# Kernel tuning notes

Measured on AMD Instinct MI355X. Metric: run time of the kernel, lower is better.

## Reference

```python
import jax, jax.numpy as jnp
import numpy as np
import math

MUL = 32          # multiplicity of 0e and 1o node irreps
NATTR = 4         # node attribute scalars (species one-hot)
NBASIS = 10       # radial basis size
HID = 64          # radial MLP hidden width
RMAX = 4.0
NUM_NEIGHBORS = 32.0
NLAYERS = 2
OUT_DIM = 16
NGRAPH = 8
SQRT3 = math.sqrt(3.0)


def smooth_cutoff(xr):
    u = 2.0 * (xr - 1.0)
    y = (1.0 - jnp.cos(math.pi * u)) * 0.5
    return jnp.where(u > 0.0, 0.0, jnp.where(u < -1.0, 1.0, y))


def fctp(s, v, attr, W0, W1, fan_in):
    # FullyConnectedTensorProduct with scalar attrs: mixes channels u x a -> w.
    norm = 1.0 / math.sqrt(fan_in)
    so = jnp.einsum('nu,na,uaw->nw', s, attr, W0) * norm
    vo = jnp.einsum('nui,na,uaw->nwi', v, attr, W1) * norm
    return so, vo


def setup_inputs() -> dict:
    key = jax.random.key(0)
    ks = jax.random.split(key, 16)
    N, E = 10000, 320000
    x = jax.random.normal(ks[0], (N, MUL * 4), dtype=jnp.float32)  # 32x0e + 32x1o
    node_attr = jax.random.uniform(ks[1], (N, NATTR), dtype=jnp.float32)
    edge_vec = jax.random.normal(ks[2], (E, 3), dtype=jnp.float32)
    edge_src = jax.random.randint(ks[3], (E,), 0, N, dtype=jnp.int32)
    edge_dst = jax.random.randint(ks[4], (E,), 0, N, dtype=jnp.int32)
    batch = jnp.sort(jax.random.randint(ks[5], (N,), 0, NGRAPH, dtype=jnp.int32))
    g = lambda k, shp: jax.random.normal(k, shp, dtype=jnp.float32)
    L = NLAYERS
    return {
        'x': x, 'node_attr': node_attr, 'edge_vec': edge_vec, 'batch': batch,
        'edge_src': edge_src, 'edge_dst': edge_dst,
        'Wsc0': g(ks[6], (L, MUL, NATTR, MUL)),
        'Wsc1': g(ks[7], (L, MUL, NATTR, MUL)),
        'Wl10': g(ks[8], (L, MUL, NATTR, MUL)),
        'Wl11': g(ks[9], (L, MUL, NATTR, MUL)),
        'Wfc1': g(ks[10], (L, NBASIS, HID)),
        'Wfc2': g(ks[11], (L, HID, 4 * MUL)),
        'Wl20': g(ks[12], (L, 2 * MUL, NATTR, MUL)),
        'Wl21': g(ks[13], (L, 2 * MUL, NATTR, MUL)),
        'Wread': g(ks[14], (MUL, NATTR, OUT_DIM)),
    }


def reference(x, node_attr, edge_vec, batch, edge_src, edge_dst,
              Wsc0, Wsc1, Wl10, Wl11, Wfc1, Wfc2, Wl20, Wl21, Wread):
    N = x.shape[0]
    s = x[:, :MUL]                                # [N, 32]  scalars (0e)
    v = x[:, MUL:].reshape(N, MUL, 3)             # [N, 32, 3] vectors (1o)

    # edge geometry -> spherical harmonics (component norm) + radial embedding
    length = jnp.linalg.norm(edge_vec, axis=-1)               # [E]
    unit = edge_vec / (length + 1e-9)[:, None]
    Y1 = SQRT3 * unit                                         # l=1 SH, Y0 == 1
    centers = jnp.linspace(0.0, RMAX, NBASIS)
    emb = jnp.exp(-(((length[:, None] - centers) / (RMAX / NBASIS)) ** 2))
    emb = emb * smooth_cutoff(length / RMAX)[:, None]         # [E, 10]

    c_s, c_x = math.sin(math.pi / 8), math.cos(math.pi / 8)

    for l in range(NLAYERS):
        # self connection and first linear (FCTP with node attrs)
        sc_s, sc_v = fctp(s, v, node_attr, Wsc0[l], Wsc1[l], MUL * NATTR)
        xs, xv = fctp(s, v, node_attr, Wl10[l], Wl11[l], MUL * NATTR)

        # radial MLP -> per-edge 'uvu' tensor-product weights (4 paths x MUL)
        h = jax.nn.silu(emb @ Wfc1[l] / math.sqrt(NBASIS))
        w = (h @ Wfc2[l]) / math.sqrt(HID)
        w = w.reshape(-1, 4, MUL)                             # [E, 4, 32]

        sE = xs[edge_src]                                     # [E, 32]
        vE = xv[edge_src]                                     # [E, 32, 3]
        # CG paths kept by Convolution (out in irreps_out or 0e):
        mid0a = w[:, 0] * sE                                   # 0e x 0e -> 0e
        mid0b = w[:, 1] * jnp.einsum('ei,eui->eu', Y1, vE) / SQRT3  # 1o x 1o -> 0e
        mid1a = w[:, 2][:, :, None] * sE[:, :, None] * Y1[:, None, :]  # 0e x 1o -> 1o
        mid1b = w[:, 3][:, :, None] * vE                       # 1o x 0e -> 1o
        mid_s = jnp.concatenate([mid0a, mid0b], axis=1)        # [E, 64]
        mid_v = jnp.concatenate([mid1a, mid1b], axis=1)        # [E, 64, 3]

        inv = 1.0 / math.sqrt(NUM_NEIGHBORS)
        agg_s = jax.ops.segment_sum(mid_s, edge_dst, num_segments=N) * inv
        agg_v = jax.ops.segment_sum(mid_v, edge_dst, num_segments=N) * inv

        os_, ov = fctp(agg_s, agg_v, node_attr, Wl20[l], Wl21[l], 2 * MUL * NATTR)
        s_new = c_s * sc_s + c_x * os_
        v_new = c_s * sc_v + c_x * ov

        # gate nonlinearity (equivariant) + residual (CustomCompose)
        s = s + jax.nn.silu(s_new)
        v = v + v_new * jax.nn.sigmoid(s_new)[:, :, None]

    # scalar readout + per-graph pooling
    out_node = jnp.einsum('nu,na,uaw->nw', s, node_attr, Wread) / math.sqrt(MUL * NATTR)
    pooled = jax.ops.segment_sum(out_node, batch, num_segments=NGRAPH)
    pooled = pooled / math.sqrt(N / NGRAPH)
    return pooled
```

## Files before the change

kernel.cpp:

```cpp
#include <hip/hip_runtime.h>
#include <math.h>

#define MUL 32
#define NATTR 4
#define NBASIS 10
#define HID 64
#define OUT_DIM 16
#define NGRAPH 8
#define NT 513

#define PI_F 3.14159265358979323846f
#define SQRT3_F 1.7320508075688772f
#define INV_SQRT3_F 0.5773502691896258f
#define INV_SQRT10_F 0.31622776601683794f
#define INV_SQRTNN_F 0.17677669529663687f
#define NORM128_F 0.08838834764831845f
#define NORM256_F 0.0625f
#define C_S_F 0.3826834323650898f
#define C_X_F 0.9238795325112867f
#define CSTEP_F (4.0f/9.0f)

__device__ inline unsigned short f2bf(float x) {
    unsigned u = __float_as_uint(x);
    u += 0x7FFF + ((u >> 16) & 1);
    return (unsigned short)(u >> 16);
}
__device__ inline float bf2f(unsigned short h) {
    return __uint_as_float(((unsigned)h) << 16);
}

__device__ __forceinline__ void init_sv_body(
    int blk, const float* __restrict__ x,
    float* __restrict__ s, float* __restrict__ v, int N) {
    int i = blk * 256 + threadIdx.x;
    if (i >= N * 128) return;
    int n = i >> 7, c = i & 127;
    float val = x[i];
    if (c < 32) s[n * 32 + c] = val;
    else        v[n * 96 + (c - 32)] = val;
}

__device__ __forceinline__ void setup_weights_body(
    int blk,
    const float* __restrict__ Wsc0, const float* __restrict__ Wl10,
    const float* __restrict__ Wsc1, const float* __restrict__ Wl11,
    const float* __restrict__ Wl20, const float* __restrict__ Wl21,
    float* __restrict__ Wfp, unsigned* __restrict__ Wupk) {
    int i = blk * 256 + threadIdx.x;
    if (i < 32768) {
        int idx = i >> 12;
        int r = i & 4095;
        int l = idx >> 2, m = idx & 3;
        const float* base = (m == 0 ? Wsc0 : m == 1 ? Wl10 : m == 2 ? Wsc1 : Wl11)
                            + l * 4096;
        int u = r >> 7, rr = r & 127, a = rr >> 5, ww = rr & 31;
        Wfp[idx * 4096 + u * 128 + ww * 4 + a] = base[r];
    } else if (i < 49152) {
        int j = i - 32768;
        int l = j >> 13;
        int r = j & 8191;
        int u = r >> 7, rr = r & 127, a = rr >> 5, ww = rr & 31;
        unsigned lo = f2bf(Wl20[l * 8192 + r]);
        unsigned hi = f2bf(Wl21[l * 8192 + r]);
        Wupk[l * 8192 + u * 128 + ww * 4 + a] = lo | (hi << 16);
    }
}

__device__ __forceinline__ void tab_gen_body(
    int blk, const float* __restrict__ Wfc1, const float* __restrict__ Wfc2,
    unsigned* __restrict__ tab, float (*sh_h)[64]) {
    int g = threadIdx.x >> 6;
    int n = threadIdx.x & 63;
    int row = blk * 4 + g;
    bool valid = row < 2 * NT;
    int l = valid ? row / NT : 0;
    int i = valid ? row % NT : 0;
    float len = (float)i * (1.0f / 128.0f);
    float uu = len * 0.5f - 2.0f;
    float cut = (uu > 0.0f) ? 0.0f
              : ((uu < -1.0f) ? 1.0f : 0.5f * (1.0f - __cosf(PI_F * uu)));
    const float* W1 = Wfc1 + l * 640;
    float a = 0.f;
#pragma unroll
    for (int k = 0; k < 10; k++) {
        float d = (len - k * CSTEP_F) * 2.5f;
        float e = __expf(-d * d) * cut;
        a += e * W1[k * 64 + n];
    }
    a *= INV_SQRT10_F;
    sh_h[g][n] = a / (1.0f + __expf(-a));
    __syncthreads();
    if (!valid) return;
    const float* W2 = Wfc2 + l * 8192;
    float w0 = 0.f, w1 = 0.f;
#pragma unroll 8
    for (int nn = 0; nn < 64; nn++) {
        float hn = sh_h[g][nn];
        w0 += hn * W2[nn * 128 + n];
        w1 += hn * W2[nn * 128 + 64 + n];
    }
    w0 *= 0.125f; w1 *= 0.125f;
    tab[(size_t)l * NT * 64 + i * 64 + n] =
        (unsigned)f2bf(w0) | ((unsigned)f2bf(w1) << 16);
}

__device__ __forceinline__ void csr_count_body(
    int blk, const int* __restrict__ edst, int* __restrict__ cnt, int E) {
    int e = blk * 256 + threadIdx.x;
    if (e < E) atomicAdd(&cnt[edst[e]], 1);
}

__device__ __forceinline__ void csr_fill_body(
    int blk, const int* __restrict__ edst, const int* __restrict__ esrc,
    const float* __restrict__ edge_vec, int* __restrict__ cursor,
    float* __restrict__ vec_csr, int E) {
    int e = blk * 256 + threadIdx.x;
    if (e < E) {
        int d = edst[e];
        int p = atomicAdd(&cursor[d], 1);
        float4 vv = {edge_vec[e * 3 + 0], edge_vec[e * 3 + 1], edge_vec[e * 3 + 2],
                     __int_as_float(esrc[e])};
        *(float4*)(vec_csr + (size_t)p * 4) = vv;
    }
}

__device__ __forceinline__ void node_fctp_body(
    int blk, int path,
    const float* __restrict__ s, const float* __restrict__ v,
    const float* __restrict__ attr, const float* __restrict__ Wfp,
    float* __restrict__ sc_s, float* __restrict__ sc_v,
    float* __restrict__ xsv, int N, char* smem) {
    float* w0 = (float*)smem;
    float* w1 = (float*)(smem + 16384);
    float (*sh)[96] = (float(*)[96])(smem + 32768);
    int ln = threadIdx.x >> 5, w = threadIdx.x & 31;
    const float4* W0p = (const float4*)(Wfp + path * 8192);
    const float4* W1p = (const float4*)(Wfp + path * 8192 + 4096);
    for (int i = threadIdx.x; i < 1024; i += 256) {
        ((float4*)w0)[i] = W0p[i];
        ((float4*)w1)[i] = W1p[i];
    }
    for (int g = 0; g < 2; g++) {
        int n = blk * 16 + g * 8 + ln;
        bool valid = n < N;
        __syncthreads();
        if (valid) {
            if (path == 0) {
                sh[ln][w] = s[n * 32 + w];
            } else {
                sh[ln][w * 3 + 0] = v[n * 96 + w * 3 + 0];
                sh[ln][w * 3 + 1] = v[n * 96 + w * 3 + 1];
                sh[ln][w * 3 + 2] = v[n * 96 + w * 3 + 2];
            }
        }
        __syncthreads();
        if (!valid) continue;
        float4 at = *(const float4*)(attr + n * 4);
        if (path == 0) {
            float acc0 = 0.f, acc1 = 0.f;
            for (int u = 0; u < 32; u++) {
                float su = sh[ln][u];
                float4 W0v = *(const float4*)(w0 + u * 128 + w * 4);
                float4 W1v = *(const float4*)(w1 + u * 128 + w * 4);
                float d0 = at.x * W0v.x + at.y * W0v.y + at.z * W0v.z + at.w * W0v.w;
                float d1 = at.x * W1v.x + at.y * W1v.y + at.z * W1v.z + at.w * W1v.w;
                acc0 += su * d0;
                acc1 += su * d1;
            }
            sc_s[n * 32 + w] = acc0 * NORM128_F;
            xsv[(size_t)n * 128 + w * 4 + 3] = acc1 * NORM128_F;
        } else {
            float a00 = 0, a01 = 0, a02 = 0, a10 = 0, a11 = 0, a12 = 0;
            for (int u = 0; u < 32; u++) {
                float vu0 = sh[ln][u * 3 + 0];
                float vu1 = sh[ln][u * 3 + 1];
                float vu2 = sh[ln][u * 3 + 2];
                float4 W0v = *(const float4*)(w0 + u * 128 + w * 4);
                float4 W1v = *(const float4*)(w1 + u * 128 + w * 4);
                float d0 = at.x * W0v.x + at.y * W0v.y + at.z * W0v.z + at.w * W0v.w;
                float d1 = at.x * W1v.x + at.y * W1v.y + at.z * W1v.z + at.w * W1v.w;
                a00 += vu0 * d0; a01 += vu1 * d0; a02 += vu2 * d0;
                a10 += vu0 * d1; a11 += vu1 * d1; a12 += vu2 * d1;
            }
            sc_v[n * 96 + w * 3 + 0] = a00 * NORM128_F;
            sc_v[n * 96 + w * 3 + 1] = a01 * NORM128_F;
            sc_v[n * 96 + w * 3 + 2] = a02 * NORM128_F;
            float* xp = xsv + (size_t)n * 128 + w * 4;
            xp[0] = a10 * NORM128_F;
            xp[1] = a11 * NORM128_F;
            xp[2] = a12 * NORM128_F;
        }
    }
}

__device__ __forceinline__ void node_update_body(
    int blk, const float* __restrict__ agg_s, const float* __restrict__ agg_v,
    const float* __restrict__ attr, const unsigned* __restrict__ Wupk,
    const float* __restrict__ sc_s, const float* __restrict__ sc_v,
    float* __restrict__ s, float* __restrict__ v, int N, char* smem) {
    unsigned* pk = (unsigned*)smem;
    float (*sh_as)[64]  = (float(*)[64])(smem + 32768);
    float (*sh_av)[192] = (float(*)[192])(smem + 32768 + 2048);
    int ln = threadIdx.x >> 5, w = threadIdx.x & 31;
    for (int i = threadIdx.x; i < 2048; i += 256)
        ((uint4*)pk)[i] = ((const uint4*)Wupk)[i];
    for (int g = 0; g < 2; g++) {
        int n = blk * 16 + g * 8 + ln;
        bool valid = n < N;
        __syncthreads();
        if (valid) {
            sh_as[ln][w] = agg_s[n * 64 + w];
            sh_as[ln][32 + w] = agg_s[n * 64 + 32 + w];
#pragma unroll
            for (int i = 0; i < 6; i++)
                sh_av[ln][w * 6 + i] = agg_v[(size_t)n * 192 + w * 6 + i];
        }
        __syncthreads();
        if (!valid) continue;
        float4 at = *(const float4*)(attr + n * 4);
        float acc_s = 0.f, a0 = 0.f, a1 = 0.f, a2 = 0.f;
        for (int u = 0; u < 64; u++) {
            float gs = sh_as[ln][u];
            float g0 = sh_av[ln][u * 3 + 0];
            float g1 = sh_av[ln][u * 3 + 1];
            float g2 = sh_av[ln][u * 3 + 2];
            uint4 pv = *(const uint4*)(pk + u * 128 + w * 4);
            float w20x = bf2f((unsigned short)pv.x), w21x = bf2f((unsigned short)(pv.x >> 16));
            float w20y = bf2f((unsigned short)pv.y), w21y = bf2f((unsigned short)(pv.y >> 16));
            float w20z = bf2f((unsigned short)pv.z), w21z = bf2f((unsigned short)(pv.z >> 16));
            float w20w = bf2f((unsigned short)pv.w), w21w = bf2f((unsigned short)(pv.w >> 16));
            float d0 = at.x * w20x + at.y * w20y + at.z * w20z + at.w * w20w;
            float d1 = at.x * w21x + at.y * w21y + at.z * w21z + at.w * w21w;
            acc_s += gs * d0;
            a0 += g0 * d1; a1 += g1 * d1; a2 += g2 * d1;
        }
        float os = acc_s * NORM256_F;
        float sn = C_S_F * sc_s[n * 32 + w] + C_X_F * os;
        float sig = 1.0f / (1.0f + __expf(-sn));
        s[n * 32 + w] += sn * sig;
        float ov0 = a0 * NORM256_F, ov1 = a1 * NORM256_F, ov2 = a2 * NORM256_F;
        v[n * 96 + w * 3 + 0] += (C_S_F * sc_v[n * 96 + w * 3 + 0] + C_X_F * ov0) * sig;
        v[n * 96 + w * 3 + 1] += (C_S_F * sc_v[n * 96 + w * 3 + 1] + C_X_F * ov1) * sig;
        v[n * 96 + w * 3 + 2] += (C_S_F * sc_v[n * 96 + w * 3 + 2] + C_X_F * ov2) * sig;
    }
}

__global__ __launch_bounds__(256) void mega1(
    int nTab, int nInit, int nSetup,
    const float* __restrict__ x, float* __restrict__ s, float* __restrict__ v,
    const float* __restrict__ Wfc1, const float* __restrict__ Wfc2,
    const float* __restrict__ Wsc0, const float* __restrict__ Wl10,
    const float* __restrict__ Wsc1, const float* __restrict__ Wl11,
    const float* __restrict__ Wl20, const float* __restrict__ Wl21,
    float* __restrict__ Wfp, unsigned* __restrict__ Wupk,
    unsigned* __restrict__ tab,
    const int* __restrict__ edst, int* __restrict__ cnt, int N, int E) {
    __shared__ float sh_h[4][64];
    int b = blockIdx.x;
    if (b < nTab) { tab_gen_body(b, Wfc1, Wfc2, tab, sh_h); return; }
    b -= nTab;
    if (b < nInit) { init_sv_body(b, x, s, v, N); return; }
    b -= nInit;
    if (b < nSetup) {
        setup_weights_body(b, Wsc0, Wl10, Wsc1, Wl11, Wl20, Wl21, Wfp, Wupk);
        return;
    }
    b -= nSetup;
    csr_count_body(b, edst, cnt, E);
}

__global__ void csr_scan(const int* __restrict__ cnt, int* __restrict__ off,
                         int* __restrict__ cursor, int N) {
    __shared__ int sums[256];
    int t = threadIdx.x;
    int chunk = (N + 255) / 256;
    int lo = t * chunk, hi = lo + chunk; if (hi > N) hi = N;
    int s = 0;
    for (int i = lo; i < hi; i++) s += cnt[i];
    sums[t] = s;
    __syncthreads();
    for (int d = 1; d < 256; d <<= 1) {
        int v = (t >= d) ? sums[t - d] : 0;
        __syncthreads();
        sums[t] += v;
        __syncthreads();
    }
    int run = (t == 0) ? 0 : sums[t - 1];
    for (int i = lo; i < hi; i++) {
        off[i] = run; cursor[i] = run;
        run += cnt[i];
    }
}

__global__ __launch_bounds__(256, 4) void mega2(
    int nFill, int nF,
    const int* __restrict__ edst, const int* __restrict__ esrc,
    const float* __restrict__ edge_vec, int* __restrict__ cursor,
    float* __restrict__ vec_csr, int E,
    const float* __restrict__ s, const float* __restrict__ v,
    const float* __restrict__ attr, const float* __restrict__ Wfp,
    float* __restrict__ sc_s, float* __restrict__ sc_v,
    float* __restrict__ xsv, int N,
    float* __restrict__ zero_base, int nZeroF4) {
    __shared__ __align__(16) char smem[35840];
    int b = blockIdx.x;
    if (b < nFill) {
        csr_fill_body(b, edst, esrc, edge_vec, cursor, vec_csr, E);
        return;
    }
    b -= nFill;
    if (b < 2 * nF) {
        node_fctp_body(b % nF, b / nF, s, v, attr, Wfp, sc_s, sc_v, xsv, N, smem);
        return;
    }
    b -= 2 * nF;
    int i = b * 256 + threadIdx.x;
    if (i < nZeroF4) {
        float4 z = {0.f, 0.f, 0.f, 0.f};
        ((float4*)zero_base)[i] = z;
    }
}

__global__ __launch_bounds__(256, 4) void gather_msgs(
    const int* __restrict__ off, const int* __restrict__ cnt,
    const unsigned* __restrict__ tab,
    const float* __restrict__ vec_csr, const float* __restrict__ xsv,
    float* __restrict__ agg_s, float* __restrict__ agg_v, int N) {
    __shared__ float red[2][8][32];
    int pair = threadIdx.x >> 7;
    int node = blockIdx.x * 2 + pair;
    int ql = threadIdx.x & 127;
    int quarter = ql >> 5;
    int u = ql & 31;
    bool active = node < N;
    int o = 0, deg = 0;
    if (active) { o = off[node]; deg = cnt[node]; }
    float as0 = 0, as1 = 0;
    float av00 = 0, av01 = 0, av02 = 0, av10 = 0, av11 = 0, av12 = 0;

    auto body = [&](int slot) {
        size_t p = (size_t)slot;
        float4 vv = *(const float4*)(vec_csr + p * 4);
        int src = __float_as_int(vv.w);
        float len = sqrtf(vv.x * vv.x + vv.y * vv.y + vv.z * vv.z);
        float rinv = SQRT3_F / (len + 1e-9f);
        float y0 = vv.x * rinv, y1 = vv.y * rinv, y2 = vv.z * rinv;
        float t = fminf(len, 3.99995f) * 128.0f;
        int ti = (int)t;
        float fr = t - (float)ti;
        const unsigned* tr = tab + ti * 64 + u;
        unsigned qa0 = tr[0],  qa1 = tr[32];
        unsigned qb0 = tr[64], qb1 = tr[96];
        float4 x4 = *(const float4*)(xsv + (size_t)src * 128 + u * 4);
        float wa0 = bf2f((unsigned short)qa0), wb0 = bf2f((unsigned short)qb0);
        float wc0 = bf2f((unsigned short)(qa0 >> 16)), wd0 = bf2f((unsigned short)(qb0 >> 16));
        float wa1 = bf2f((unsigned short)qa1), wb1 = bf2f((unsigned short)qb1);
        float wc1 = bf2f((unsigned short)(qa1 >> 16)), wd1 = bf2f((unsigned short)(qb1 >> 16));
        float wa = wa0 + fr * (wb0 - wa0);
        float wc = wc0 + fr * (wd0 - wc0);
        float wb = wa1 + fr * (wb1 - wa1);
        float wd = wc1 + fr * (wd1 - wc1);
        as0 += wa * x4.w;
        as1 += wb * (y0 * x4.x + y1 * x4.y + y2 * x4.z) * INV_SQRT3_F;
        float tt = wc * x4.w;
        av00 += tt * y0;  av01 += tt * y1;  av02 += tt * y2;
        av10 += wd * x4.x; av11 += wd * x4.y; av12 += wd * x4.z;
    };

    int i = quarter;
    for (; i + 4 < deg; i += 8) { body(o + i); body(o + i + 4); }
    for (; i < deg; i += 4) body(o + i);

    as0 += __shfl_down(as0, 32);  as1 += __shfl_down(as1, 32);
    av00 += __shfl_down(av00, 32); av01 += __shfl_down(av01, 32); av02 += __shfl_down(av02, 32);
    av10 += __shfl_down(av10, 32); av11 += __shfl_down(av11, 32); av12 += __shfl_down(av12, 32);

    int lane = threadIdx.x & 63;
    int upper_wave = (threadIdx.x >> 6) & 1;
    if (upper_wave && lane < 32) {
        red[pair][0][u] = as0;  red[pair][1][u] = as1;
        red[pair][2][u] = av00; red[pair][3][u] = av01; red[pair][4][u] = av02;
        red[pair][5][u] = av10; red[pair][6][u] = av11; red[pair][7][u] = av12;
    }
    __syncthreads();
    if (active && !upper_wave && lane < 32) {
        as0  += red[pair][0][u];  as1  += red[pair][1][u];
        av00 += red[pair][2][u];  av01 += red[pair][3][u];  av02 += red[pair][4][u];
        av10 += red[pair][5][u];  av11 += red[pair][6][u];  av12 += red[pair][7][u];
        agg_s[node * 64 + u]      = as0 * INV_SQRTNN_F;
        agg_s[node * 64 + 32 + u] = as1 * INV_SQRTNN_F;
        float* av = agg_v + (size_t)node * 192;
        av[u * 3 + 0]      = av00 * INV_SQRTNN_F;
        av[u * 3 + 1]      = av01 * INV_SQRTNN_F;
        av[u * 3 + 2]      = av02 * INV_SQRTNN_F;
        av[96 + u * 3 + 0] = av10 * INV_SQRTNN_F;
        av[96 + u * 3 + 1] = av11 * INV_SQRTNN_F;
        av[96 + u * 3 + 2] = av12 * INV_SQRTNN_F;
    }
}

__global__ __launch_bounds__(256, 4) void update_fctp(
    const float* __restrict__ agg_s, const float* __restrict__ agg_v,
    const float* __restrict__ attr, const unsigned* __restrict__ Wupk,
    float* __restrict__ sc_s, float* __restrict__ sc_v,
    float* __restrict__ s, float* __restrict__ v,
    const float* __restrict__ Wfp_next, float* __restrict__ xsv,
    int N, int do_fctp) {
    __shared__ __align__(16) char smem[40960];
    node_update_body(blockIdx.x, agg_s, agg_v, attr, Wupk, sc_s, sc_v, s, v, N, smem);
    if (do_fctp) {
        __syncthreads();
        node_fctp_body(blockIdx.x, 0, s, v, attr, Wfp_next, sc_s, sc_v, xsv, N, smem);
        __syncthreads();
        node_fctp_body(blockIdx.x, 1, s, v, attr, Wfp_next, sc_s, sc_v, xsv, N, smem);
    }
}

__global__ __launch_bounds__(256) void readout(
    const float* __restrict__ s, const float* __restrict__ attr,
    const float* __restrict__ Wread, const int* __restrict__ batch,
    float* __restrict__ out, int N, float pool_scale) {
    __shared__ float wr[2048];
    __shared__ float red[NGRAPH * 16];
    for (int i = threadIdx.x; i < 2048; i += 256) wr[i] = Wread[i];
    if (threadIdx.x < NGRAPH * 16) red[threadIdx.x] = 0.f;
    __syncthreads();
    int ln = threadIdx.x >> 4, w = threadIdx.x & 15;
    for (int g = 0; g < 4; g++) {
        int n = blockIdx.x * 64 + g * 16 + ln;
        if (n < N) {
            float4 at = *(const float4*)(attr + n * 4);
            float fa[4] = {at.x, at.y, at.z, at.w};
            float acc = 0.f;
            for (int u = 0; u < 32; u++) {
                float su = s[n * 32 + u];
                int base = u * 64 + w;
#pragma unroll
                for (int a = 0; a < 4; a++) acc += su * fa[a] * wr[base + a * 16];
            }
            atomicAdd(&red[batch[n] * 16 + w], acc);
        }
    }
    __syncthreads();
    if (threadIdx.x < NGRAPH * 16) {
        float val = red[threadIdx.x];
        if (val != 0.f)
            atomicAdd(&out[threadIdx.x], val * NORM128_F * pool_scale);
    }
}

extern "C" void kernel_launch(void* const* d_in, const int* in_sizes, int n_in,
                              void* d_out, int out_size, void* d_ws, size_t ws_size,
                              hipStream_t stream) {
    const float* x        = (const float*)d_in[0];
    const float* nattr    = (const float*)d_in[1];
    const float* edge_vec = (const float*)d_in[2];
    const int*   batch    = (const int*)d_in[3];
    const int*   esrc     = (const int*)d_in[4];
    const int*   edst     = (const int*)d_in[5];
    const float* Wsc0  = (const float*)d_in[6];
    const float* Wsc1  = (const float*)d_in[7];
    const float* Wl10  = (const float*)d_in[8];
    const float* Wl11  = (const float*)d_in[9];
    const float* Wfc1  = (const float*)d_in[10];
    const float* Wfc2  = (const float*)d_in[11];
    const float* Wl20  = (const float*)d_in[12];
    const float* Wl21  = (const float*)d_in[13];
    const float* Wread = (const float*)d_in[14];

    int N = in_sizes[0] / (MUL * 4);
    int E = in_sizes[2] / 3;

    float* p = (float*)d_ws;
    float* vec_csr = p; p += (size_t)E * 4;
    unsigned* tab = (unsigned*)p; p += 2 * NT * 64;
    float* Wfp    = p; p += 32768;
    unsigned* Wupk = (unsigned*)p; p += 16384;
    float* s_buf  = p; p += (size_t)N * 32;
    float* v_buf  = p; p += (size_t)N * 96;
    float* sc_s   = p; p += (size_t)N * 32;
    float* sc_v   = p; p += (size_t)N * 96;
    float* xsv    = p; p += (size_t)N * 128;
    float* aggA_s = p; p += (size_t)N * 64;
    float* aggA_v = p; p += (size_t)N * 192;
    float* aggB_s = p; p += (size_t)N * 64;
    float* aggB_v = p; p += (size_t)N * 192;
    int* cnt     = (int*)p; p += N;
    int* off     = (int*)p; p += N;
    int* cursor  = (int*)p; p += N;

    hipMemsetAsync(d_out, 0, (size_t)out_size * sizeof(float), stream);
    hipMemsetAsync(cnt, 0, (size_t)N * sizeof(int), stream);

    int nTab   = (2 * NT + 3) / 4;
    int nInit  = (N * 128 + 255) / 256;
    int nSetup = 192;
    int nCount = (E + 255) / 256;
    mega1<<<nTab + nInit + nSetup + nCount, 256, 0, stream>>>(
        nTab, nInit, nSetup, x, s_buf, v_buf,
        Wfc1, Wfc2, Wsc0, Wl10, Wsc1, Wl11, Wl20, Wl21,
        Wfp, Wupk, tab, edst, cnt, N, E);

    csr_scan<<<1, 256, 0, stream>>>(cnt, off, cursor, N);

    int nFill = (E + 255) / 256;
    int nF = (N + 15) / 16;
    int nZeroF4 = N * 128;
    int nZeroBlk = (nZeroF4 + 255) / 256;
    mega2<<<nFill + 2 * nF + nZeroBlk, 256, 0, stream>>>(
        nFill, nF, edst, esrc, edge_vec, cursor, vec_csr, E,
        s_buf, v_buf, nattr, Wfp, sc_s, sc_v, xsv, N, aggA_s, nZeroF4);

    int nG = (N + 1) / 2;

    gather_msgs<<<nG, 256, 0, stream>>>(
        off, cnt, tab, vec_csr, xsv, aggA_s, aggA_v, N);
    update_fctp<<<nF, 256, 0, stream>>>(
        aggA_s, aggA_v, nattr, Wupk, sc_s, sc_v, s_buf, v_buf,
        Wfp + 16384, xsv, N, 1);

    gather_msgs<<<nG, 256, 0, stream>>>(
        off, cnt, tab + NT * 64, vec_csr, xsv, aggB_s, aggB_v, N);
    update_fctp<<<nF, 256, 0, stream>>>(
        aggB_s, aggB_v, nattr, Wupk + 8192, sc_s, sc_v, s_buf, v_buf,
        (const float*)0, xsv, N, 0);

    float pool_scale = (float)(1.0 / sqrt((double)N / (double)NGRAPH));
    readout<<<(N + 63) / 64, 256, 0, stream>>>(
        s_buf, nattr, Wread, batch, (float*)d_out, N, pool_scale);
}
```

Measured before the change: 291.9 us.

## Fuse node update into gather kernel and drop aggregate buffers

The per-node message gather now finishes its reduction in shared memory and applies the Wl2 tensor product, gate and residual update in the same kernel, so the agg_s/agg_v intermediate buffers, their zeroing pass and the separate update launches go away. The next layer's node fctp runs as its own kernel. This removes a global round trip of the aggregates and some launches. In exchange the update loop runs on only one wave per node (32 lanes), reads weights straight from global memory instead of staging them in LDS, and may lengthen the gather kernel.

```diff
diff --git a/kernel.cpp b/kernel.cpp
--- a/kernel.cpp
+++ b/kernel.cpp
@@ -193,58 +193,6 @@
     }
 }
 
-__device__ __forceinline__ void node_update_body(
-    int blk, const float* __restrict__ agg_s, const float* __restrict__ agg_v,
-    const float* __restrict__ attr, const unsigned* __restrict__ Wupk,
-    const float* __restrict__ sc_s, const float* __restrict__ sc_v,
-    float* __restrict__ s, float* __restrict__ v, int N, char* smem) {
-    unsigned* pk = (unsigned*)smem;
-    float (*sh_as)[64]  = (float(*)[64])(smem + 32768);
-    float (*sh_av)[192] = (float(*)[192])(smem + 32768 + 2048);
-    int ln = threadIdx.x >> 5, w = threadIdx.x & 31;
-    for (int i = threadIdx.x; i < 2048; i += 256)
-        ((uint4*)pk)[i] = ((const uint4*)Wupk)[i];
-    for (int g = 0; g < 2; g++) {
-        int n = blk * 16 + g * 8 + ln;
-        bool valid = n < N;
-        __syncthreads();
-        if (valid) {
-            sh_as[ln][w] = agg_s[n * 64 + w];
-            sh_as[ln][32 + w] = agg_s[n * 64 + 32 + w];
-#pragma unroll
-            for (int i = 0; i < 6; i++)
-                sh_av[ln][w * 6 + i] = agg_v[(size_t)n * 192 + w * 6 + i];
-        }
-        __syncthreads();
-        if (!valid) continue;
-        float4 at = *(const float4*)(attr + n * 4);
-        float acc_s = 0.f, a0 = 0.f, a1 = 0.f, a2 = 0.f;
-        for (int u = 0; u < 64; u++) {
-            float gs = sh_as[ln][u];
-            float g0 = sh_av[ln][u * 3 + 0];
-            float g1 = sh_av[ln][u * 3 + 1];
-            float g2 = sh_av[ln][u * 3 + 2];
-            uint4 pv = *(const uint4*)(pk + u * 128 + w * 4);
-            float w20x = bf2f((unsigned short)pv.x), w21x = bf2f((unsigned short)(pv.x >> 16));
-            float w20y = bf2f((unsigned short)pv.y), w21y = bf2f((unsigned short)(pv.y >> 16));
-            float w20z = bf2f((unsigned short)pv.z), w21z = bf2f((unsigned short)(pv.z >> 16));
-            float w20w = bf2f((unsigned short)pv.w), w21w = bf2f((unsigned short)(pv.w >> 16));
-            float d0 = at.x * w20x + at.y * w20y + at.z * w20z + at.w * w20w;
-            float d1 = at.x * w21x + at.y * w21y + at.z * w21z + at.w * w21w;
-            acc_s += gs * d0;
-            a0 += g0 * d1; a1 += g1 * d1; a2 += g2 * d1;
-        }
-        float os = acc_s * NORM256_F;
-        float sn = C_S_F * sc_s[n * 32 + w] + C_X_F * os;
-        float sig = 1.0f / (1.0f + __expf(-sn));
-        s[n * 32 + w] += sn * sig;
-        float ov0 = a0 * NORM256_F, ov1 = a1 * NORM256_F, ov2 = a2 * NORM256_F;
-        v[n * 96 + w * 3 + 0] += (C_S_F * sc_v[n * 96 + w * 3 + 0] + C_X_F * ov0) * sig;
-        v[n * 96 + w * 3 + 1] += (C_S_F * sc_v[n * 96 + w * 3 + 1] + C_X_F * ov1) * sig;
-        v[n * 96 + w * 3 + 2] += (C_S_F * sc_v[n * 96 + w * 3 + 2] + C_X_F * ov2) * sig;
-    }
-}
-
 __global__ __launch_bounds__(256) void mega1(
     int nTab, int nInit, int nSetup,
     const float* __restrict__ x, float* __restrict__ s, float* __restrict__ v,
@@ -300,8 +248,7 @@
     const float* __restrict__ s, const float* __restrict__ v,
     const float* __restrict__ attr, const float* __restrict__ Wfp,
     float* __restrict__ sc_s, float* __restrict__ sc_v,
-    float* __restrict__ xsv, int N,
-    float* __restrict__ zero_base, int nZeroF4) {
+    float* __restrict__ xsv, int N) {
     __shared__ __align__(16) char smem[35840];
     int b = blockIdx.x;
     if (b < nFill) {
@@ -309,23 +256,27 @@
         return;
     }
     b -= nFill;
-    if (b < 2 * nF) {
-        node_fctp_body(b % nF, b / nF, s, v, attr, Wfp, sc_s, sc_v, xsv, N, smem);
-        return;
-    }
-    b -= 2 * nF;
-    int i = b * 256 + threadIdx.x;
-    if (i < nZeroF4) {
-        float4 z = {0.f, 0.f, 0.f, 0.f};
-        ((float4*)zero_base)[i] = z;
-    }
-}
-
-__global__ __launch_bounds__(256, 4) void gather_msgs(
+    node_fctp_body(b % nF, b / nF, s, v, attr, Wfp, sc_s, sc_v, xsv, N, smem);
+}
+
+__global__ __launch_bounds__(256, 4) void fctp_only(
+    int nF,
+    const float* __restrict__ s, const float* __restrict__ v,
+    const float* __restrict__ attr, const float* __restrict__ Wfp,
+    float* __restrict__ sc_s, float* __restrict__ sc_v,
+    float* __restrict__ xsv, int N) {
+    __shared__ __align__(16) char smem[35840];
+    node_fctp_body(blockIdx.x % nF, blockIdx.x / nF, s, v, attr, Wfp,
+                   sc_s, sc_v, xsv, N, smem);
+}
+
+__global__ __launch_bounds__(256, 4) void gather_update(
     const int* __restrict__ off, const int* __restrict__ cnt,
     const unsigned* __restrict__ tab,
     const float* __restrict__ vec_csr, const float* __restrict__ xsv,
-    float* __restrict__ agg_s, float* __restrict__ agg_v, int N) {
+    const float* __restrict__ attr, const unsigned* __restrict__ Wupk,
+    const float* __restrict__ sc_s, const float* __restrict__ sc_v,
+    float* __restrict__ s, float* __restrict__ v, int N) {
     __shared__ float red[2][8][32];
     int pair = threadIdx.x >> 7;
     int node = blockIdx.x * 2 + pair;
@@ -383,36 +334,50 @@
         red[pair][5][u] = av10; red[pair][6][u] = av11; red[pair][7][u] = av12;
     }
     __syncthreads();
-    if (active && !upper_wave && lane < 32) {
-        as0  += red[pair][0][u];  as1  += red[pair][1][u];
-        av00 += red[pair][2][u];  av01 += red[pair][3][u];  av02 += red[pair][4][u];
-        av10 += red[pair][5][u];  av11 += red[pair][6][u];  av12 += red[pair][7][u];
-        agg_s[node * 64 + u]      = as0 * INV_SQRTNN_F;
-        agg_s[node * 64 + 32 + u] = as1 * INV_SQRTNN_F;
-        float* av = agg_v + (size_t)node * 192;
-        av[u * 3 + 0]      = av00 * INV_SQRTNN_F;
-        av[u * 3 + 1]      = av01 * INV_SQRTNN_F;
-        av[u * 3 + 2]      = av02 * INV_SQRTNN_F;
-        av[96 + u * 3 + 0] = av10 * INV_SQRTNN_F;
-        av[96 + u * 3 + 1] = av11 * INV_SQRTNN_F;
-        av[96 + u * 3 + 2] = av12 * INV_SQRTNN_F;
-    }
-}
-
-__global__ __launch_bounds__(256, 4) void update_fctp(
-    const float* __restrict__ agg_s, const float* __restrict__ agg_v,
-    const float* __restrict__ attr, const unsigned* __restrict__ Wupk,
-    float* __restrict__ sc_s, float* __restrict__ sc_v,
-    float* __restrict__ s, float* __restrict__ v,
-    const float* __restrict__ Wfp_next, float* __restrict__ xsv,
-    int N, int do_fctp) {
-    __shared__ __align__(16) char smem[40960];
-    node_update_body(blockIdx.x, agg_s, agg_v, attr, Wupk, sc_s, sc_v, s, v, N, smem);
-    if (do_fctp) {
-        __syncthreads();
-        node_fctp_body(blockIdx.x, 0, s, v, attr, Wfp_next, sc_s, sc_v, xsv, N, smem);
-        __syncthreads();
-        node_fctp_body(blockIdx.x, 1, s, v, attr, Wfp_next, sc_s, sc_v, xsv, N, smem);
+    if (!upper_wave && lane < 32) {
+        red[pair][0][u] = (as0 + red[pair][0][u]) * INV_SQRTNN_F;
+        red[pair][1][u] = (as1 + red[pair][1][u]) * INV_SQRTNN_F;
+        red[pair][2][u] = (av00 + red[pair][2][u]) * INV_SQRTNN_F;
+        red[pair][3][u] = (av01 + red[pair][3][u]) * INV_SQRTNN_F;
+        red[pair][4][u] = (av02 + red[pair][4][u]) * INV_SQRTNN_F;
+        red[pair][5][u] = (av10 + red[pair][5][u]) * INV_SQRTNN_F;
+        red[pair][6][u] = (av11 + red[pair][6][u]) * INV_SQRTNN_F;
+        red[pair][7][u] = (av12 + red[pair][7][u]) * INV_SQRTNN_F;
+    }
+    __syncthreads();
+
+    if (active && quarter == 0) {
+        int w = u;
+        float4 at = *(const float4*)(attr + node * 4);
+        float acc_s = 0.f, a0 = 0.f, a1 = 0.f, a2 = 0.f;
+#pragma unroll 8
+        for (int uu = 0; uu < 64; uu++) {
+            float gs, g0, g1, g2;
+            if (uu < 32) {
+                gs = red[pair][0][uu];
+                g0 = red[pair][2][uu]; g1 = red[pair][3][uu]; g2 = red[pair][4][uu];
+            } else {
+                gs = red[pair][1][uu - 32];
+                g0 = red[pair][5][uu - 32]; g1 = red[pair][6][uu - 32]; g2 = red[pair][7][uu - 32];
+            }
+            uint4 pv = *(const uint4*)(Wupk + uu * 128 + w * 4);
+            float w20x = bf2f((unsigned short)pv.x), w21x = bf2f((unsigned short)(pv.x >> 16));
+            float w20y = bf2f((unsigned short)pv.y), w21y = bf2f((unsigned short)(pv.y >> 16));
+            float w20z = bf2f((unsigned short)pv.z), w21z = bf2f((unsigned short)(pv.z >> 16));
+            float w20w = bf2f((unsigned short)pv.w), w21w = bf2f((unsigned short)(pv.w >> 16));
+            float d0 = at.x * w20x + at.y * w20y + at.z * w20z + at.w * w20w;
+            float d1 = at.x * w21x + at.y * w21y + at.z * w21z + at.w * w21w;
+            acc_s += gs * d0;
+            a0 += g0 * d1; a1 += g1 * d1; a2 += g2 * d1;
+        }
+        float os = acc_s * NORM256_F;
+        float sn = C_S_F * sc_s[node * 32 + w] + C_X_F * os;
+        float sig = 1.0f / (1.0f + __expf(-sn));
+        s[node * 32 + w] += sn * sig;
+        float ov0 = a0 * NORM256_F, ov1 = a1 * NORM256_F, ov2 = a2 * NORM256_F;
+        v[node * 96 + w * 3 + 0] += (C_S_F * sc_v[node * 96 + w * 3 + 0] + C_X_F * ov0) * sig;
+        v[node * 96 + w * 3 + 1] += (C_S_F * sc_v[node * 96 + w * 3 + 1] + C_X_F * ov1) * sig;
+        v[node * 96 + w * 3 + 2] += (C_S_F * sc_v[node * 96 + w * 3 + 2] + C_X_F * ov2) * sig;
     }
 }
 
@@ -481,10 +446,6 @@
     float* sc_s   = p; p += (size_t)N * 32;
     float* sc_v   = p; p += (size_t)N * 96;
     float* xsv    = p; p += (size_t)N * 128;
-    float* aggA_s = p; p += (size_t)N * 64;
-    float* aggA_v = p; p += (size_t)N * 192;
-    float* aggB_s = p; p += (size_t)N * 64;
-    float* aggB_v = p; p += (size_t)N * 192;
     int* cnt     = (int*)p; p += N;
     int* off     = (int*)p; p += N;
     int* cursor  = (int*)p; p += N;
@@ -505,25 +466,21 @@
 
     int nFill = (E + 255) / 256;
     int nF = (N + 15) / 16;
-    int nZeroF4 = N * 128;
-    int nZeroBlk = (nZeroF4 + 255) / 256;
-    mega2<<<nFill + 2 * nF + nZeroBlk, 256, 0, stream>>>(
+    mega2<<<nFill + 2 * nF, 256, 0, stream>>>(
         nFill, nF, edst, esrc, edge_vec, cursor, vec_csr, E,
-        s_buf, v_buf, nattr, Wfp, sc_s, sc_v, xsv, N, aggA_s, nZeroF4);
+        s_buf, v_buf, nattr, Wfp, sc_s, sc_v, xsv, N);
 
     int nG = (N + 1) / 2;
 
-    gather_msgs<<<nG, 256, 0, stream>>>(
-        off, cnt, tab, vec_csr, xsv, aggA_s, aggA_v, N);
-    update_fctp<<<nF, 256, 0, stream>>>(
-        aggA_s, aggA_v, nattr, Wupk, sc_s, sc_v, s_buf, v_buf,
-        Wfp + 16384, xsv, N, 1);
-
-    gather_msgs<<<nG, 256, 0, stream>>>(
-        off, cnt, tab + NT * 64, vec_csr, xsv, aggB_s, aggB_v, N);
-    update_fctp<<<nF, 256, 0, stream>>>(
-        aggB_s, aggB_v, nattr, Wupk + 8192, sc_s, sc_v, s_buf, v_buf,
-        (const float*)0, xsv, N, 0);
+    gather_update<<<nG, 256, 0, stream>>>(
+        off, cnt, tab, vec_csr, xsv, nattr, Wupk,
+        sc_s, sc_v, s_buf, v_buf, N);
+    fctp_only<<<2 * nF, 256, 0, stream>>>(
+        nF, s_buf, v_buf, nattr, Wfp + 16384, sc_s, sc_v, xsv, N);
+
+    gather_update<<<nG, 256, 0, stream>>>(
+        off, cnt, tab + NT * 64, vec_csr, xsv, nattr, Wupk + 8192,
+        sc_s, sc_v, s_buf, v_buf, N);
 
     float pool_scale = (float)(1.0 / sqrt((double)N / (double)NGRAPH));
     readout<<<(N + 63) / 64, 256, 0, stream>>>(
```

Measured after the change: 308.3 us. 5.6% more time.
